# Optimization experiments

Hardware: AMD Instinct MI355X
Metric: run time of the kernel (lower is better)

The kernel has to match this reference:

```python
import jax, jax.numpy as jnp
import numpy as np

N_PAIRS = 1_000_000
N_OBJS = 1000
X_DIM = 48


def setup_inputs() -> dict:
    key = jax.random.key(0)
    ks = jax.random.split(key, 10)
    return {
        "o1": jax.random.randint(ks[0], (N_PAIRS,), 0, N_OBJS, dtype=jnp.int64 if jax.config.jax_enable_x64 else jnp.int32),
        "o2": jax.random.randint(ks[1], (N_PAIRS,), 0, N_OBJS, dtype=jnp.int64 if jax.config.jax_enable_x64 else jnp.int32),
        "T": jax.random.normal(ks[2], (N_PAIRS, 4, 4), dtype=jnp.float32),
        "geoms": jax.random.normal(ks[3], (N_OBJS, X_DIM), dtype=jnp.float32),
        "W1": jax.random.normal(ks[4], (96, 96), dtype=jnp.float32) * 0.1,
        "b1": jax.random.normal(ks[5], (96,), dtype=jnp.float32) * 0.1,
        "W2": jax.random.normal(ks[6], (96, 96), dtype=jnp.float32) * 0.1,
        "b2": jax.random.normal(ks[7], (96,), dtype=jnp.float32) * 0.1,
        "W3": jax.random.normal(ks[8], (96, 1), dtype=jnp.float32) * 0.1,
        "b3": jax.random.normal(ks[9], (1,), dtype=jnp.float32) * 0.1,
    }


def _apply_transforms(x, T):
    # x: [N, D] treated as D//3 3-vectors; homogeneous transform by T [N,4,4].
    N, D = x.shape
    v = x.reshape(N, D // 3, 3)
    # R @ v + t  (equivalent to appending 1 and taking first 3 rows of T)
    out = jnp.einsum('nij,nxj->nxi', T[:, :3, :3], v) + T[:, :3, 3][:, None, :]
    return out.reshape(N, D)


def _mlp(x, W1, b1, W2, b2, W3, b3):
    h = jax.nn.relu(x @ W1 + b1)
    h = jax.nn.relu(h @ W2 + b2)
    return (h @ W3 + b3)[:, 0]  # squeeze -> [N]


def reference(o1, o2, T, geoms, W1, b1, W2, b2, W3, b3):
    x1 = geoms[o1]          # [N, 48]
    x2 = geoms[o2]          # [N, 48]

    def branch(a, b, Tm):
        bt = _apply_transforms(b, Tm)
        x = jnp.concatenate([a, bt], axis=1)  # [N, 96]
        return _mlp(x, W1, b1, W2, b2, W3, b3)

    d_1_2 = branch(x1, x2, T)
    T_inv = jnp.linalg.inv(T)
    d_2_1 = branch(x2, x1, T_inv)
    return 0.5 * (d_1_2 + d_2_1)
```

## Files before the change

kernel.cpp:

```cpp
#include <hip/hip_runtime.h>
#include <hip/hip_bf16.h>

typedef __attribute__((ext_vector_type(8))) short bf16x8;
typedef __attribute__((ext_vector_type(4))) float f32x4;

constexpr int BT   = 1024;
constexpr int KD   = 96;
constexpr int LDX  = 104;
constexpr int LDT  = 12;
constexpr int NBLK = 256;
constexpr int TOTW = NBLK * (BT / 64);

constexpr size_t GBF_BYTES = 48000 * 2;

__device__ inline ushort f2bf(float f) {
    uint u = __float_as_uint(f);
    u += 0x7fffu + ((u >> 16) & 1u);
    return (ushort)(u >> 16);
}

__device__ inline uint f2bf2(float lo, float hi) {
    float2 t; t.x = lo; t.y = hi;
    __hip_bfloat162 h = __float22bfloat162_rn(t);
    union { __hip_bfloat162 b; uint u; } cv;
    cv.b = h;
    return cv.u;
}

__global__ void prep_geoms(const float* __restrict__ g, ushort* __restrict__ gb, int n) {
    int i = blockIdx.x * 256 + threadIdx.x;
    if (i < n) gb[i] = f2bf(g[i]);
}

__device__ inline void inv4x4(float4 t0, float4 t1, float4 t2, float4 t3,
                              float* __restrict__ ti) {
    double m00=t0.x, m01=t0.y, m02=t0.z, m03=t0.w;
    double m10=t1.x, m11=t1.y, m12=t1.z, m13=t1.w;
    double m20=t2.x, m21=t2.y, m22=t2.z, m23=t2.w;
    double m30=t3.x, m31=t3.y, m32=t3.z, m33=t3.w;
    double A2323 = m22*m33 - m23*m32;
    double A1323 = m21*m33 - m23*m31;
    double A1223 = m21*m32 - m22*m31;
    double A0323 = m20*m33 - m23*m30;
    double A0223 = m20*m32 - m22*m30;
    double A0123 = m20*m31 - m21*m30;
    double A2313 = m12*m33 - m13*m32;
    double A1313 = m11*m33 - m13*m31;
    double A1213 = m11*m32 - m12*m31;
    double A2312 = m12*m23 - m13*m22;
    double A1312 = m11*m23 - m13*m21;
    double A1212 = m11*m22 - m12*m21;
    double A0313 = m10*m33 - m13*m30;
    double A0213 = m10*m32 - m12*m30;
    double A0312 = m10*m23 - m13*m20;
    double A0212 = m10*m22 - m12*m20;
    double A0113 = m10*m31 - m11*m30;
    double A0112 = m10*m21 - m11*m20;
    double det = m00*(m11*A2323 - m12*A1323 + m13*A1223)
               - m01*(m10*A2323 - m12*A0323 + m13*A0223)
               + m02*(m10*A1323 - m11*A0323 + m13*A0123)
               - m03*(m10*A1223 - m11*A0223 + m12*A0123);
    double idet = 1.0 / det;
    ti[0]  = (float)( idet *  (m11*A2323 - m12*A1323 + m13*A1223) );
    ti[1]  = (float)( idet * -(m01*A2323 - m02*A1323 + m03*A1223) );
    ti[2]  = (float)( idet *  (m01*A2313 - m02*A1313 + m03*A1213) );
    ti[3]  = (float)( idet * -(m01*A2312 - m02*A1312 + m03*A1212) );
    ti[4]  = (float)( idet * -(m10*A2323 - m12*A0323 + m13*A0223) );
    ti[5]  = (float)( idet *  (m00*A2323 - m02*A0323 + m03*A0223) );
    ti[6]  = (float)( idet * -(m00*A2313 - m02*A0313 + m03*A0213) );
    ti[7]  = (float)( idet *  (m00*A2312 - m02*A0312 + m03*A0212) );
    ti[8]  = (float)( idet *  (m10*A1323 - m11*A0323 + m13*A0123) );
    ti[9]  = (float)( idet * -(m00*A1323 - m01*A0323 + m03*A0123) );
    ti[10] = (float)( idet *  (m00*A1313 - m01*A0313 + m03*A0113) );
    ti[11] = (float)( idet * -(m00*A1312 - m01*A0312 + m03*A0112) );
}

__global__ void __launch_bounds__(256) prep_tinv(const float* __restrict__ Tg,
                                                 float* __restrict__ tg, int N) {
    int i = blockIdx.x * 256 + threadIdx.x;
    if (i >= N) return;
    const float4* T4 = reinterpret_cast<const float4*>(Tg + (size_t)i * 16);
    float4 t0 = T4[0], t1 = T4[1], t2 = T4[2], t3 = T4[3];
    float ti[12];
    inv4x4(t0, t1, t2, t3, ti);
    float4* dst = reinterpret_cast<float4*>(tg + (size_t)i * 12);
    dst[0] = *reinterpret_cast<float4*>(&ti[0]);
    dst[1] = *reinterpret_cast<float4*>(&ti[4]);
    dst[2] = *reinterpret_cast<float4*>(&ti[8]);
}

template<int PREINV>
__global__ void __launch_bounds__(BT, 4) collision_mfma(
    const int* __restrict__ o1, const int* __restrict__ o2,
    const float* __restrict__ Tg, const float* __restrict__ geoms,
    const ushort* __restrict__ gbf, const float* __restrict__ tinvg,
    const float* __restrict__ W1, const float* __restrict__ b1,
    const float* __restrict__ W2, const float* __restrict__ b2,
    const float* __restrict__ W3, const float* __restrict__ b3,
    float* __restrict__ out, int N)
{
    __shared__ ushort xs[512 * LDX];
    __shared__ ushort wlds[36 * 64 * 8];
    __shared__ float  bls[292];
    __shared__ float  tinv[PREINV ? 4 : 256 * LDT];

    const int tid = threadIdx.x;
    const int w   = tid >> 6;
    const int l   = tid & 63;
    const int cl  = l & 15;
    const int g   = l >> 4;
    const int rg  = g * 4;

    const int rl = l & 31;
    const int pt = l >> 5;
    const int br = rl >> 4;
    const int dp = rl & 15;

    for (int e = tid; e < 36 * 512; e += BT) {
        int f    = e >> 9;
        int r    = e & 511;
        int lane = r >> 3;
        int j    = r & 7;
        int L    = f / 18;
        int fr   = f - L * 18;
        int mt   = fr / 3;
        int kb   = fr - mt * 3;
        int gg   = lane >> 4;
        int cc   = lane & 15;
        const float* W = L ? W2 : W1;
        wlds[e] = f2bf(W[(kb * 32 + gg * 8 + j) * KD + mt * 16 + cc]);
    }
    if (tid < 96) {
        bls[tid]       = b1[tid];
        bls[96 + tid]  = b2[tid];
        bls[192 + tid] = W3[tid];
    }
    if (tid == 96) bls[288] = b3[0];
    __syncthreads();

    const int NWT = N >> 4;
    const int gw  = blockIdx.x * (BT / 64) + w;

    for (int wt = gw; wt < NWT; wt += TOTW) {
        const int pbase = wt * 16;

        uint off0 = 0;
        asm volatile("" : "+v"(off0));
        const ushort* wp = wlds + off0;
        const float*  bp = bls + off0;

        if constexpr (!PREINV) {
            if (l < 16) {
                const float4* T4 = reinterpret_cast<const float4*>(Tg + (size_t)(pbase + l) * 16);
                float4 t0 = T4[0], t1 = T4[1], t2 = T4[2], t3 = T4[3];
                inv4x4(t0, t1, t2, t3, &tinv[(w * 16 + l) * LDT]);
            }
        }

        {
            const int p  = pbase + dp;
            const int ia = o1[p], ib = o2[p];
            const int oa = br ? ib : ia;
            const int ob = br ? ia : ib;
            ushort* xrow = xs + (w * 32 + rl) * LDX;

            {
                const uint4* src = reinterpret_cast<const uint4*>(gbf + oa * 48 + pt * 24);
                uint4* dst = reinterpret_cast<uint4*>(xrow + pt * 24);
                dst[0] = src[0]; dst[1] = src[1]; dst[2] = src[2];
            }

            float4 M0, M1, M2;
            if (br == 0) {
                const float4* Tp = reinterpret_cast<const float4*>(Tg + (size_t)p * 16);
                M0 = Tp[0]; M1 = Tp[1]; M2 = Tp[2];
            } else {
                if constexpr (PREINV) {
                    const float4* t4 = reinterpret_cast<const float4*>(tinvg + (size_t)p * 12);
                    M0 = t4[0]; M1 = t4[1]; M2 = t4[2];
                } else {
                    const float4* t4 = reinterpret_cast<const float4*>(&tinv[(w * 16 + dp) * LDT]);
                    M0 = t4[0]; M1 = t4[1]; M2 = t4[2];
                }
            }
            float v[24];
            {
                const float4* bs = reinterpret_cast<const float4*>(geoms + (size_t)ob * 48 + pt * 24);
                #pragma unroll
                for (int q = 0; q < 6; ++q) {
                    float4 t = bs[q];
                    v[4*q+0] = t.x; v[4*q+1] = t.y; v[4*q+2] = t.z; v[4*q+3] = t.w;
                }
            }
            float o[24];
            #pragma unroll
            for (int m = 0; m < 8; ++m) {
                float vx = v[3*m+0], vy = v[3*m+1], vz = v[3*m+2];
                o[3*m+0] = fmaf(M0.x, vx, fmaf(M0.y, vy, fmaf(M0.z, vz, M0.w)));
                o[3*m+1] = fmaf(M1.x, vx, fmaf(M1.y, vy, fmaf(M1.z, vz, M1.w)));
                o[3*m+2] = fmaf(M2.x, vx, fmaf(M2.y, vy, fmaf(M2.z, vz, M2.w)));
            }
            union { uint u[12]; uint4 q4[3]; } pk;
            #pragma unroll
            for (int q = 0; q < 12; ++q)
                pk.u[q] = f2bf2(o[2*q], o[2*q+1]);
            uint4* dst = reinterpret_cast<uint4*>(xrow + 48 + pt * 24);
            dst[0] = pk.q4[0]; dst[1] = pk.q4[1]; dst[2] = pk.q4[2];
        }

        f32x4 acc[6][2];
        #pragma unroll
        for (int mt = 0; mt < 6; ++mt) {
            f32x4 bv = *reinterpret_cast<const f32x4*>(bp + mt*16 + rg);
            acc[mt][0] = bv;
            acc[mt][1] = bv;
        }
        bf16x8 xf[2][3];
        #pragma unroll
        for (int nt = 0; nt < 2; ++nt)
            #pragma unroll
            for (int kb = 0; kb < 3; ++kb)
                xf[nt][kb] = *reinterpret_cast<const bf16x8*>(
                    xs + (w*32 + nt*16 + cl) * LDX + kb*32 + g*8);
        #pragma unroll
        for (int mt = 0; mt < 6; ++mt) {
            bf16x8 wfr[3];
            #pragma unroll
            for (int kb = 0; kb < 3; ++kb)
                wfr[kb] = *reinterpret_cast<const bf16x8*>(
                    wp + ((0*18 + mt*3 + kb) * 64 + l) * 8);
            #pragma unroll
            for (int nt = 0; nt < 2; ++nt)
                #pragma unroll
                for (int kb = 0; kb < 3; ++kb)
                    acc[mt][nt] = __builtin_amdgcn_mfma_f32_16x16x32_bf16(
                        wfr[kb], xf[nt][kb], acc[mt][nt], 0, 0, 0);
        }

        #pragma unroll
        for (int mt = 0; mt < 6; ++mt) {
            #pragma unroll
            for (int nt = 0; nt < 2; ++nt) {
                uint2 u2;
                u2.x = f2bf2(fmaxf(acc[mt][nt][0], 0.f), fmaxf(acc[mt][nt][1], 0.f));
                u2.y = f2bf2(fmaxf(acc[mt][nt][2], 0.f), fmaxf(acc[mt][nt][3], 0.f));
                *reinterpret_cast<uint2*>(
                    xs + (w*32 + nt*16 + cl) * LDX + mt*16 + rg) = u2;
            }
        }

        f32x4 acc2[6][2];
        #pragma unroll
        for (int mt = 0; mt < 6; ++mt) {
            f32x4 bv = *reinterpret_cast<const f32x4*>(bp + 96 + mt*16 + rg);
            acc2[mt][0] = bv;
            acc2[mt][1] = bv;
        }
        bf16x8 hf[2][3];
        #pragma unroll
        for (int nt = 0; nt < 2; ++nt)
            #pragma unroll
            for (int kb = 0; kb < 3; ++kb)
                hf[nt][kb] = *reinterpret_cast<const bf16x8*>(
                    xs + (w*32 + nt*16 + cl) * LDX + kb*32 + g*8);
        #pragma unroll
        for (int mt = 0; mt < 6; ++mt) {
            bf16x8 wfr[3];
            #pragma unroll
            for (int kb = 0; kb < 3; ++kb)
                wfr[kb] = *reinterpret_cast<const bf16x8*>(
                    wp + ((1*18 + mt*3 + kb) * 64 + l) * 8);
            #pragma unroll
            for (int nt = 0; nt < 2; ++nt)
                #pragma unroll
                for (int kb = 0; kb < 3; ++kb)
                    acc2[mt][nt] = __builtin_amdgcn_mfma_f32_16x16x32_bf16(
                        wfr[kb], hf[nt][kb], acc2[mt][nt], 0, 0, 0);
        }

        float pr0 = 0.f, pr1 = 0.f;
        #pragma unroll
        for (int mt = 0; mt < 6; ++mt) {
            f32x4 w3v = *reinterpret_cast<const f32x4*>(bp + 192 + mt*16 + rg);
            pr0 = fmaf(fmaxf(acc2[mt][0][0], 0.f), w3v[0], pr0);
            pr0 = fmaf(fmaxf(acc2[mt][0][1], 0.f), w3v[1], pr0);
            pr0 = fmaf(fmaxf(acc2[mt][0][2], 0.f), w3v[2], pr0);
            pr0 = fmaf(fmaxf(acc2[mt][0][3], 0.f), w3v[3], pr0);
            pr1 = fmaf(fmaxf(acc2[mt][1][0], 0.f), w3v[0], pr1);
            pr1 = fmaf(fmaxf(acc2[mt][1][1], 0.f), w3v[1], pr1);
            pr1 = fmaf(fmaxf(acc2[mt][1][2], 0.f), w3v[2], pr1);
            pr1 = fmaf(fmaxf(acc2[mt][1][3], 0.f), w3v[3], pr1);
        }
        pr0 += __shfl_xor(pr0, 16, 64);
        pr0 += __shfl_xor(pr0, 32, 64);
        pr1 += __shfl_xor(pr1, 16, 64);
        pr1 += __shfl_xor(pr1, 32, 64);
        if (l < 16)
            out[pbase + l] = 0.5f * (pr0 + pr1) + bp[288];
    }
}

extern "C" void kernel_launch(void* const* d_in, const int* in_sizes, int n_in,
                              void* d_out, int out_size, void* d_ws, size_t ws_size,
                              hipStream_t stream) {
    const int*   o1    = (const int*)d_in[0];
    const int*   o2    = (const int*)d_in[1];
    const float* T     = (const float*)d_in[2];
    const float* geoms = (const float*)d_in[3];
    const float* W1    = (const float*)d_in[4];
    const float* b1    = (const float*)d_in[5];
    const float* W2    = (const float*)d_in[6];
    const float* b2    = (const float*)d_in[7];
    const float* W3    = (const float*)d_in[8];
    const float* b3    = (const float*)d_in[9];
    float* out = (float*)d_out;
    const int N  = in_sizes[0];
    const int NG = in_sizes[3];

    ushort* gbf   = (ushort*)d_ws;
    float*  tinvg = (float*)((char*)d_ws + GBF_BYTES);
    const bool pre = ws_size >= GBF_BYTES + (size_t)N * 12 * sizeof(float);

    hipLaunchKernelGGL(prep_geoms, dim3((NG + 255) / 256), dim3(256), 0, stream,
                       geoms, gbf, NG);
    if (pre) {
        hipLaunchKernelGGL(prep_tinv, dim3((N + 255) / 256), dim3(256), 0, stream,
                           T, tinvg, N);
        hipLaunchKernelGGL((collision_mfma<1>), dim3(NBLK), dim3(BT), 0, stream,
                           o1, o2, T, geoms, gbf, tinvg,
                           W1, b1, W2, b2, W3, b3, out, N);
    } else {
        hipLaunchKernelGGL((collision_mfma<0>), dim3(NBLK), dim3(BT), 0, stream,
                           o1, o2, T, geoms, gbf, (const float*)nullptr,
                           W1, b1, W2, b2, W3, b3, out, N);
    }
}
```

Before: 143.2 us.

## Fuse 4x4 transform inversion into main kernel prologue, drop separate prep kernel

Removes the standalone prep_tinv launch. In a prologue of the MLP kernel, each wave inverts the transforms for the tiles it will later process and writes them to the workspace. The goal is to cut one launch and its full pass over T, and to keep the inverted transforms warm in cache for the main loop. In exchange the prologue covers at most 16 tiles per wave, so larger N would leave inverses uncomputed. It also depends on intra-wave global write-then-read visibility without an explicit fence.

```diff
diff --git a/kernel.cpp b/kernel.cpp
--- a/kernel.cpp
+++ b/kernel.cpp
@@ -75,25 +75,11 @@
     ti[11] = (float)( idet * -(m00*A1312 - m01*A0312 + m03*A0112) );
 }
 
-__global__ void __launch_bounds__(256) prep_tinv(const float* __restrict__ Tg,
-                                                 float* __restrict__ tg, int N) {
-    int i = blockIdx.x * 256 + threadIdx.x;
-    if (i >= N) return;
-    const float4* T4 = reinterpret_cast<const float4*>(Tg + (size_t)i * 16);
-    float4 t0 = T4[0], t1 = T4[1], t2 = T4[2], t3 = T4[3];
-    float ti[12];
-    inv4x4(t0, t1, t2, t3, ti);
-    float4* dst = reinterpret_cast<float4*>(tg + (size_t)i * 12);
-    dst[0] = *reinterpret_cast<float4*>(&ti[0]);
-    dst[1] = *reinterpret_cast<float4*>(&ti[4]);
-    dst[2] = *reinterpret_cast<float4*>(&ti[8]);
-}
-
 template<int PREINV>
 __global__ void __launch_bounds__(BT, 4) collision_mfma(
     const int* __restrict__ o1, const int* __restrict__ o2,
     const float* __restrict__ Tg, const float* __restrict__ geoms,
-    const ushort* __restrict__ gbf, const float* __restrict__ tinvg,
+    const ushort* __restrict__ gbf, float* __restrict__ tinvg,
     const float* __restrict__ W1, const float* __restrict__ b1,
     const float* __restrict__ W2, const float* __restrict__ b2,
     const float* __restrict__ W3, const float* __restrict__ b3,
@@ -140,6 +126,25 @@
 
     const int NWT = N >> 4;
     const int gw  = blockIdx.x * (BT / 64) + w;
+
+    if constexpr (PREINV) {
+        for (int it = 0; it < 4; ++it) {
+            if ((size_t)gw + (size_t)(it * 4) * TOTW >= (size_t)NWT) break;
+            const int k  = it * 4 + (l >> 4);
+            const int wt = gw + k * TOTW;
+            if (wt < NWT) {
+                const int p = wt * 16 + (l & 15);
+                const float4* T4 = reinterpret_cast<const float4*>(Tg + (size_t)p * 16);
+                float4 t0 = T4[0], t1 = T4[1], t2 = T4[2], t3 = T4[3];
+                float tl[12];
+                inv4x4(t0, t1, t2, t3, tl);
+                float4* dst = reinterpret_cast<float4*>(tinvg + (size_t)p * 12);
+                dst[0] = *reinterpret_cast<float4*>(&tl[0]);
+                dst[1] = *reinterpret_cast<float4*>(&tl[4]);
+                dst[2] = *reinterpret_cast<float4*>(&tl[8]);
+            }
+        }
+    }
 
     for (int wt = gw; wt < NWT; wt += TOTW) {
         const int pbase = wt * 16;
@@ -324,14 +329,12 @@
     hipLaunchKernelGGL(prep_geoms, dim3((NG + 255) / 256), dim3(256), 0, stream,
                        geoms, gbf, NG);
     if (pre) {
-        hipLaunchKernelGGL(prep_tinv, dim3((N + 255) / 256), dim3(256), 0, stream,
-                           T, tinvg, N);
         hipLaunchKernelGGL((collision_mfma<1>), dim3(NBLK), dim3(BT), 0, stream,
                            o1, o2, T, geoms, gbf, tinvg,
                            W1, b1, W2, b2, W3, b3, out, N);
     } else {
         hipLaunchKernelGGL((collision_mfma<0>), dim3(NBLK), dim3(BT), 0, stream,
-                           o1, o2, T, geoms, gbf, (const float*)nullptr,
+                           o1, o2, T, geoms, gbf, (float*)nullptr,
                            W1, b1, W2, b2, W3, b3, out, N);
     }
 }
```

Result: faster. 138.0 us (-3.6%).
